# Optimization experiments

Measured on AMD Instinct MI355X. Metric: run time of the kernel, lower is better.

The kernel has to match this reference:

```python
import jax, jax.numpy as jnp
import numpy as np

# Module config (mirrors init_kwargs)
B = 131072          # batch of trajectories
N_STATES = 16       # n_x_f + n_x_b
N_SEL = 8           # states selected per subnet (band width of Binary_mat)
N_U = 4             # inputs
N_FEAT = 64         # hidden width, neuron_list = [64, 64]
N_OUT = 16          # n_x_o, one output per subnet

# Binary_mat[i, j] = 1 iff (j - i) mod 16 < 8. The torch loop collects selected
# indices in INCREASING j order, so sort each row's selected set.
IDX = np.sort((np.arange(N_OUT)[:, None] + np.arange(N_SEL)[None, :]) % N_STATES, axis=1)  # [16, 8] int


def setup_inputs() -> dict:
    key = jax.random.key(0)
    k0, k1, k2, k3, k4, k5 = jax.random.split(key, 6)
    zin = N_SEL + N_U  # 12 = per-subnet MLP input width
    return {
        "x_f": jax.random.normal(k0, (B, 8), jnp.float32),
        "x_b": jax.random.normal(k1, (B, 8), jnp.float32),
        "u": jax.random.normal(k2, (B, N_U), jnp.float32),
        # stacked per-subnet weights (nn.Linear stores [out, in]); no biases
        "W0": jax.random.normal(k3, (N_OUT, N_FEAT, zin), jnp.float32) * 0.05,
        "W1": jax.random.normal(k4, (N_OUT, N_FEAT, N_FEAT), jnp.float32) * 0.05,
        "W2": jax.random.normal(k5, (N_OUT, 1, N_FEAT), jnp.float32) * 0.05,
    }


def reference(x_f, x_b, u, W0, W1, W2):
    # x_tilde = cat(x_f, x_b): [B, 16]
    x_tilde = jnp.concatenate([x_f, x_b], axis=-1)
    # Per-subnet gather of its selected state subset: [B, 16(sub), 8]
    x_sel = x_tilde[:, IDX]
    # Append exogenous input u to every subnet's input: [B, 16, 12]
    u_b = jnp.broadcast_to(u[:, None, :], (u.shape[0], N_OUT, N_U))
    z = jnp.concatenate([x_sel, u_b], axis=-1)
    # Grouped small MLPs (Linear+Tanh, Linear+Tanh, Linear) as batched GEMMs
    h = jnp.tanh(jnp.einsum('bsi,soi->bso', z, W0))   # [B, 16, 64]
    h = jnp.tanh(jnp.einsum('bsh,soh->bso', h, W1))   # [B, 16, 64]
    dx = jnp.einsum('bsh,soh->bso', h, W2)[..., 0]    # scatter into dx slices -> [B, 16]
    return dx
```

## Files before the change

kernel.cpp:

```cpp
#include <hip/hip_runtime.h>


#define N_STATES 16
#define CHUNK    8

typedef _Float16 f16x8 __attribute__((ext_vector_type(8)));
typedef float    f32x4 __attribute__((ext_vector_type(4)));
typedef __fp16   h2    __attribute__((ext_vector_type(2)));

__device__ __forceinline__ h2 pack2(float a, float b) {
    return __builtin_amdgcn_cvt_pkrtz(a, b);
}
__device__ __forceinline__ unsigned int h2_bits(h2 v) {
    union { h2 h; unsigned int u; } x; x.h = v; return x.u;
}
__device__ __forceinline__ f16x8 u4_to_h8(uint4 v) {
    union { uint4 u; f16x8 h; } x; x.u = v; return x.h;
}
__device__ __forceinline__ uint4 h8_to_u4(f16x8 h) {
    union { f16x8 h; uint4 u; } x; x.h = h; return x.u;
}

__device__ __forceinline__ h2 tanh_pk(h2 x) {
    const h2 hi = {(__fp16)1.25f, (__fp16)1.25f};
    const h2 lo = {(__fp16)-1.25f, (__fp16)-1.25f};
    x = __builtin_elementwise_min(__builtin_elementwise_max(x, lo), hi);
    h2 s = x * x;
    const h2 c4 = {(__fp16)0.00598591f, (__fp16)0.00598591f};
    const h2 c3 = {(__fp16)-0.03807894f, (__fp16)-0.03807894f};
    const h2 c2 = {(__fp16)0.12576901f, (__fp16)0.12576901f};
    const h2 c1 = {(__fp16)-0.33203310f, (__fp16)-0.33203310f};
    const h2 c0 = {(__fp16)0.99998110f, (__fp16)0.99998110f};
    h2 p = s * c4 + c3;
    p = s * p + c2;
    p = s * p + c1;
    p = s * p + c0;
    return x * p;
}

__global__ __launch_bounds__(256, 4) void fans_mfma_kernel(
    const float* __restrict__ x_f, const float* __restrict__ x_b,
    const float* __restrict__ u,   const float* __restrict__ W0,
    const float* __restrict__ W1,  const float* __restrict__ W2,
    float* __restrict__ out)
{
    __shared__ __align__(16) uint4 zplA[256];
    __shared__ __align__(16) uint2 zplB[256];
    __shared__ __align__(16) unsigned int Hd[4][16][36];
    __shared__ __align__(16) uint4 sA0[4][32];

    const int s   = blockIdx.y;
    const int tid = threadIdx.x;
    const int b0  = blockIdx.x * (256 * CHUNK);

    const int lid = tid & 63;
    const int w   = tid >> 6;
    const int c   = lid & 15;
    const int q   = lid >> 4;

    if (tid < 64 && q < 2) {
        const float* w0s = W0 + s * 768;
        #pragma unroll
        for (int t = 0; t < 4; ++t) {
            f16x8 v;
            #pragma unroll
            for (int j = 0; j < 8; ++j) {
                const int k = 8 * q + j;
                v[j] = (_Float16)((k < 12) ? w0s[(16 * t + c) * 12 + k] : 0.0f);
            }
            sA0[t][lid] = h8_to_u4(v);
        }
    }

    f16x8 a1[2][4];
    {
        const float* w1s = W1 + s * 4096;
        #pragma unroll
        for (int ks = 0; ks < 2; ++ks) {
            #pragma unroll
            for (int t = 0; t < 4; ++t) {
                const float4* p = (const float4*)(w1s + (16 * t + c) * 64 + 32 * ks + 8 * q);
                const float4 v0 = p[0], v1 = p[1];
                a1[ks][t] = (f16x8){(_Float16)v0.x, (_Float16)v0.y, (_Float16)v0.z, (_Float16)v0.w,
                                    (_Float16)v1.x, (_Float16)v1.y, (_Float16)v1.z, (_Float16)v1.w};
            }
        }
    }
    h2 w2p[8];
    {
        const float* w2s = W2 + s * 64;
        #pragma unroll
        for (int t = 0; t < 4; ++t) {
            const int base = 16 * t + 4 * q;
            w2p[2 * t + 0] = pack2(w2s[base + 0], w2s[base + 1]);
            w2p[2 * t + 1] = pack2(w2s[base + 2], w2s[base + 3]);
        }
    }

    __syncthreads();

    const int wrap = (s > 8) ? (s - 8) : 0;

    #pragma unroll 1
    for (int ch = 0; ch < CHUNK; ++ch) {
        const int rbase = b0 + ch * 256;

        {
            const int row = rbase + tid;
            float zs[8];
            #pragma unroll
            for (int j = 0; j < 8; ++j) {
                const int idx = (j < wrap) ? j : (s + j - wrap);
                zs[j] = (idx < 8) ? x_f[row * 8 + idx] : x_b[row * 8 + (idx - 8)];
            }
            const float4 uv = *(const float4*)(u + row * 4);
            zplA[tid] = make_uint4(h2_bits(pack2(zs[0], zs[1])), h2_bits(pack2(zs[2], zs[3])),
                                   h2_bits(pack2(zs[4], zs[5])), h2_bits(pack2(zs[6], zs[7])));
            zplB[tid] = make_uint2(h2_bits(pack2(uv.x, uv.y)), h2_bits(pack2(uv.z, uv.w)));
        }

        #pragma unroll
        for (int m = 0; m < 4; ++m) {
            const int rowb = 64 * w + 16 * m;

            f16x8 zf = {0, 0, 0, 0, 0, 0, 0, 0};
            if (q == 0) {
                zf = u4_to_h8(zplA[rowb + c]);
            } else if (q == 1) {
                const uint2 b = zplB[rowb + c];
                zf = u4_to_h8(make_uint4(b.x, b.y, 0u, 0u));
            }

            f32x4 c1[4];
            #pragma unroll
            for (int t = 0; t < 4; ++t) {
                f16x8 a0t = {0, 0, 0, 0, 0, 0, 0, 0};
                if (q < 2) a0t = u4_to_h8(sA0[t][lid]);
                c1[t] = __builtin_amdgcn_mfma_f32_16x16x32_f16(
                    a0t, zf, (f32x4){0.f, 0.f, 0.f, 0.f}, 0, 0, 0);
            }

            #pragma unroll
            for (int t = 0; t < 4; ++t) {
                const h2 th0 = tanh_pk(pack2(c1[t][0], c1[t][1]));
                const h2 th1 = tanh_pk(pack2(c1[t][2], c1[t][3]));
                *(uint2*)&Hd[w][c][8 * t + 2 * q] = make_uint2(h2_bits(th0), h2_bits(th1));
            }

            f32x4 c2[4] = {{0.f, 0.f, 0.f, 0.f}, {0.f, 0.f, 0.f, 0.f},
                           {0.f, 0.f, 0.f, 0.f}, {0.f, 0.f, 0.f, 0.f}};
            #pragma unroll
            for (int ks = 0; ks < 2; ++ks) {
                const f16x8 hb = u4_to_h8(*(const uint4*)&Hd[w][c][16 * ks + 4 * q]);
                #pragma unroll
                for (int t = 0; t < 4; ++t)
                    c2[t] = __builtin_amdgcn_mfma_f32_16x16x32_f16(a1[ks][t], hb, c2[t], 0, 0, 0);
            }

            float ar0 = 0.f, ar1 = 0.f;
            #pragma unroll
            for (int t = 0; t < 4; ++t) {
                const h2 th0 = tanh_pk(pack2(c2[t][0], c2[t][1]));
                const h2 th1 = tanh_pk(pack2(c2[t][2], c2[t][3]));
                ar0 = __builtin_amdgcn_fdot2(th0, w2p[2 * t + 0], ar0, false);
                ar1 = __builtin_amdgcn_fdot2(th1, w2p[2 * t + 1], ar1, false);
            }
            float acc = ar0 + ar1;
            acc += __shfl_xor(acc, 16);
            acc += __shfl_xor(acc, 32);

            if (lid < 16)
                out[(rbase + rowb + lid) * N_STATES + s] = acc;
        }
    }
}

extern "C" void kernel_launch(void* const* d_in, const int* in_sizes, int n_in,
                              void* d_out, int out_size, void* d_ws, size_t ws_size,
                              hipStream_t stream) {
    const float* x_f = (const float*)d_in[0];
    const float* x_b = (const float*)d_in[1];
    const float* u   = (const float*)d_in[2];
    const float* W0  = (const float*)d_in[3];
    const float* W1  = (const float*)d_in[4];
    const float* W2  = (const float*)d_in[5];
    float* out = (float*)d_out;

    const int nb = in_sizes[0] / 8;
    dim3 grid(nb / (256 * CHUNK), N_STATES);
    fans_mfma_kernel<<<grid, 256, 0, stream>>>(x_f, x_b, u, W0, W1, W2, out);
}
```

Baseline: 139.1 us.

## Switch MLP layers to 32x32x16 MFMA tiles with register-resident W0

Replaces the 16x16x32 f16 MFMA tiling with 32x32x16 tiles, processing 32 rows per step instead of 16. Layer 1 now uses K=16, which cuts the zero-padding waste in the 12-wide first layer. W0 fragments are loaded directly into registers, which removes the shared-memory staging and the block barrier, and the final reduction needs one fewer shuffle. The cost is larger accumulator register pressure (f32x16) and a reworked hidden-activation layout in shared memory that may raise bank conflicts.

```diff
diff --git a/kernel.cpp b/kernel.cpp
--- a/kernel.cpp
+++ b/kernel.cpp
@@ -4,9 +4,9 @@
 #define N_STATES 16
 #define CHUNK    8
 
-typedef _Float16 f16x8 __attribute__((ext_vector_type(8)));
-typedef float    f32x4 __attribute__((ext_vector_type(4)));
-typedef __fp16   h2    __attribute__((ext_vector_type(2)));
+typedef _Float16 f16x8  __attribute__((ext_vector_type(8)));
+typedef float    f32x16 __attribute__((ext_vector_type(16)));
+typedef __fp16   h2     __attribute__((ext_vector_type(2)));
 
 __device__ __forceinline__ h2 pack2(float a, float b) {
     return __builtin_amdgcn_cvt_pkrtz(a, b);
@@ -16,9 +16,6 @@
 }
 __device__ __forceinline__ f16x8 u4_to_h8(uint4 v) {
     union { uint4 u; f16x8 h; } x; x.u = v; return x.h;
-}
-__device__ __forceinline__ uint4 h8_to_u4(f16x8 h) {
-    union { f16x8 h; uint4 u; } x; x.h = h; return x.u;
 }
 
 __device__ __forceinline__ h2 tanh_pk(h2 x) {
@@ -46,8 +43,7 @@
 {
     __shared__ __align__(16) uint4 zplA[256];
     __shared__ __align__(16) uint2 zplB[256];
-    __shared__ __align__(16) unsigned int Hd[4][16][36];
-    __shared__ __align__(16) uint4 sA0[4][32];
+    __shared__ __align__(16) unsigned int Hd[4][32][36];
 
     const int s   = blockIdx.y;
     const int tid = threadIdx.x;
@@ -55,49 +51,54 @@
 
     const int lid = tid & 63;
     const int w   = tid >> 6;
-    const int c   = lid & 15;
-    const int q   = lid >> 4;
+    const int n   = lid & 31;
+    const int h   = lid >> 5;
 
-    if (tid < 64 && q < 2) {
+    f16x8 a0[2];
+    {
         const float* w0s = W0 + s * 768;
         #pragma unroll
-        for (int t = 0; t < 4; ++t) {
+        for (int Mh = 0; Mh < 2; ++Mh) {
+            const float* base = w0s + (32 * Mh + n) * 12;
             f16x8 v;
-            #pragma unroll
-            for (int j = 0; j < 8; ++j) {
-                const int k = 8 * q + j;
-                v[j] = (_Float16)((k < 12) ? w0s[(16 * t + c) * 12 + k] : 0.0f);
+            if (h == 0) {
+                const float4 v0 = *(const float4*)(base + 0);
+                const float4 v1 = *(const float4*)(base + 4);
+                v = (f16x8){(_Float16)v0.x, (_Float16)v0.y, (_Float16)v0.z, (_Float16)v0.w,
+                            (_Float16)v1.x, (_Float16)v1.y, (_Float16)v1.z, (_Float16)v1.w};
+            } else {
+                const float4 v0 = *(const float4*)(base + 8);
+                v = (f16x8){(_Float16)v0.x, (_Float16)v0.y, (_Float16)v0.z, (_Float16)v0.w,
+                            (_Float16)0.f, (_Float16)0.f, (_Float16)0.f, (_Float16)0.f};
             }
-            sA0[t][lid] = h8_to_u4(v);
+            a0[Mh] = v;
         }
     }
-
     f16x8 a1[2][4];
     {
         const float* w1s = W1 + s * 4096;
         #pragma unroll
-        for (int ks = 0; ks < 2; ++ks) {
+        for (int Mh = 0; Mh < 2; ++Mh) {
             #pragma unroll
-            for (int t = 0; t < 4; ++t) {
-                const float4* p = (const float4*)(w1s + (16 * t + c) * 64 + 32 * ks + 8 * q);
+            for (int kc = 0; kc < 4; ++kc) {
+                const float4* p = (const float4*)(w1s + (32 * Mh + n) * 64 + 16 * kc + 8 * h);
                 const float4 v0 = p[0], v1 = p[1];
-                a1[ks][t] = (f16x8){(_Float16)v0.x, (_Float16)v0.y, (_Float16)v0.z, (_Float16)v0.w,
-                                    (_Float16)v1.x, (_Float16)v1.y, (_Float16)v1.z, (_Float16)v1.w};
+                a1[Mh][kc] = (f16x8){(_Float16)v0.x, (_Float16)v0.y, (_Float16)v0.z, (_Float16)v0.w,
+                                     (_Float16)v1.x, (_Float16)v1.y, (_Float16)v1.z, (_Float16)v1.w};
             }
         }
     }
-    h2 w2p[8];
+    h2 w2p[16];
     {
         const float* w2s = W2 + s * 64;
         #pragma unroll
-        for (int t = 0; t < 4; ++t) {
-            const int base = 16 * t + 4 * q;
-            w2p[2 * t + 0] = pack2(w2s[base + 0], w2s[base + 1]);
-            w2p[2 * t + 1] = pack2(w2s[base + 2], w2s[base + 3]);
-        }
+        for (int Mh = 0; Mh < 2; ++Mh)
+            #pragma unroll
+            for (int k = 0; k < 8; ++k) {
+                const int f = 32 * Mh + 8 * (k >> 1) + 2 * (k & 1) + 4 * h;
+                w2p[8 * Mh + k] = pack2(w2s[f], w2s[f + 1]);
+            }
     }
-
-    __syncthreads();
 
     const int wrap = (s > 8) ? (s - 8) : 0;
 
@@ -120,57 +121,55 @@
         }
 
         #pragma unroll
-        for (int m = 0; m < 4; ++m) {
-            const int rowb = 64 * w + 16 * m;
+        for (int m = 0; m < 2; ++m) {
+            const int rowb = 64 * w + 32 * m;
 
-            f16x8 zf = {0, 0, 0, 0, 0, 0, 0, 0};
-            if (q == 0) {
-                zf = u4_to_h8(zplA[rowb + c]);
-            } else if (q == 1) {
-                const uint2 b = zplB[rowb + c];
+            f16x8 zf;
+            if (h == 0) {
+                zf = u4_to_h8(zplA[rowb + n]);
+            } else {
+                const uint2 b = zplB[rowb + n];
                 zf = u4_to_h8(make_uint4(b.x, b.y, 0u, 0u));
             }
 
-            f32x4 c1[4];
+            const f32x16 z16 = {0.f,0.f,0.f,0.f,0.f,0.f,0.f,0.f,
+                                0.f,0.f,0.f,0.f,0.f,0.f,0.f,0.f};
+            f32x16 c1a = __builtin_amdgcn_mfma_f32_32x32x16_f16(a0[0], zf, z16, 0, 0, 0);
+            f32x16 c1b = __builtin_amdgcn_mfma_f32_32x32x16_f16(a0[1], zf, z16, 0, 0, 0);
+
             #pragma unroll
-            for (int t = 0; t < 4; ++t) {
-                f16x8 a0t = {0, 0, 0, 0, 0, 0, 0, 0};
-                if (q < 2) a0t = u4_to_h8(sA0[t][lid]);
-                c1[t] = __builtin_amdgcn_mfma_f32_16x16x32_f16(
-                    a0t, zf, (f32x4){0.f, 0.f, 0.f, 0.f}, 0, 0, 0);
+            for (int a = 0; a < 4; ++a) {
+                const int r = 4 * a;
+                *(uint2*)&Hd[w][n][16 * 0 + 4 * a + 2 * h] =
+                    make_uint2(h2_bits(tanh_pk(pack2(c1a[r], c1a[r + 1]))),
+                               h2_bits(tanh_pk(pack2(c1a[r + 2], c1a[r + 3]))));
+                *(uint2*)&Hd[w][n][16 * 1 + 4 * a + 2 * h] =
+                    make_uint2(h2_bits(tanh_pk(pack2(c1b[r], c1b[r + 1]))),
+                               h2_bits(tanh_pk(pack2(c1b[r + 2], c1b[r + 3]))));
             }
 
+            f32x16 c2a = z16, c2b = z16;
             #pragma unroll
-            for (int t = 0; t < 4; ++t) {
-                const h2 th0 = tanh_pk(pack2(c1[t][0], c1[t][1]));
-                const h2 th1 = tanh_pk(pack2(c1[t][2], c1[t][3]));
-                *(uint2*)&Hd[w][c][8 * t + 2 * q] = make_uint2(h2_bits(th0), h2_bits(th1));
-            }
-
-            f32x4 c2[4] = {{0.f, 0.f, 0.f, 0.f}, {0.f, 0.f, 0.f, 0.f},
-                           {0.f, 0.f, 0.f, 0.f}, {0.f, 0.f, 0.f, 0.f}};
-            #pragma unroll
-            for (int ks = 0; ks < 2; ++ks) {
-                const f16x8 hb = u4_to_h8(*(const uint4*)&Hd[w][c][16 * ks + 4 * q]);
-                #pragma unroll
-                for (int t = 0; t < 4; ++t)
-                    c2[t] = __builtin_amdgcn_mfma_f32_16x16x32_f16(a1[ks][t], hb, c2[t], 0, 0, 0);
+            for (int kc = 0; kc < 4; ++kc) {
+                const f16x8 hb = u4_to_h8(*(const uint4*)&Hd[w][n][8 * kc + 4 * h]);
+                c2a = __builtin_amdgcn_mfma_f32_32x32x16_f16(a1[0][kc], hb, c2a, 0, 0, 0);
+                c2b = __builtin_amdgcn_mfma_f32_32x32x16_f16(a1[1][kc], hb, c2b, 0, 0, 0);
             }
 
             float ar0 = 0.f, ar1 = 0.f;
             #pragma unroll
-            for (int t = 0; t < 4; ++t) {
-                const h2 th0 = tanh_pk(pack2(c2[t][0], c2[t][1]));
-                const h2 th1 = tanh_pk(pack2(c2[t][2], c2[t][3]));
-                ar0 = __builtin_amdgcn_fdot2(th0, w2p[2 * t + 0], ar0, false);
-                ar1 = __builtin_amdgcn_fdot2(th1, w2p[2 * t + 1], ar1, false);
+            for (int a = 0; a < 4; ++a) {
+                const int r = 4 * a;
+                ar0 = __builtin_amdgcn_fdot2(tanh_pk(pack2(c2a[r], c2a[r + 1])), w2p[2 * a + 0], ar0, false);
+                ar0 = __builtin_amdgcn_fdot2(tanh_pk(pack2(c2a[r + 2], c2a[r + 3])), w2p[2 * a + 1], ar0, false);
+                ar1 = __builtin_amdgcn_fdot2(tanh_pk(pack2(c2b[r], c2b[r + 1])), w2p[8 + 2 * a + 0], ar1, false);
+                ar1 = __builtin_amdgcn_fdot2(tanh_pk(pack2(c2b[r + 2], c2b[r + 3])), w2p[8 + 2 * a + 1], ar1, false);
             }
             float acc = ar0 + ar1;
-            acc += __shfl_xor(acc, 16);
             acc += __shfl_xor(acc, 32);
 
-            if (lid < 16)
-                out[(rbase + rowb + lid) * N_STATES + s] = acc;
+            if (lid < 32)
+                out[(rbase + rowb + n) * N_STATES + s] = acc;
         }
     }
 }
```

After: 128.2 us. 1.09x faster.
